# Kernel optimization log

Hardware: AMD Instinct MI355X
Metric: run time of the kernel (lower is better)

Reference implementation:

```python
import jax, jax.numpy as jnp
import numpy as np

N_NODES = 50000
N_EDGES = 800000
IN_CH = 128
HID = 64
OUT_CH = 10
N_GRAPHS = 512


def setup_inputs() -> dict:
    key = jax.random.key(0)
    ks = jax.random.split(key, 16)
    x = jax.random.normal(ks[0], (N_NODES, IN_CH), dtype=jnp.float32)
    edge_index = jax.random.randint(ks[1], (2, N_EDGES), 0, N_NODES, dtype=jnp.int64)
    batch = jnp.sort(jax.random.randint(ks[2], (N_NODES,), 0, N_GRAPHS, dtype=jnp.int64))
    def lin(k, fan_in, fan_out):
        bound = 1.0 / np.sqrt(fan_in)
        kw, kb = jax.random.split(k)
        w = jax.random.uniform(kw, (fan_in, fan_out), minval=-bound, maxval=bound, dtype=jnp.float32)
        b = jax.random.uniform(kb, (fan_out,), minval=-bound, maxval=bound, dtype=jnp.float32)
        return w, b
    w0a, b0a = lin(ks[3], IN_CH, HID)
    w0b, b0b = lin(ks[4], HID, HID)
    w1a, b1a = lin(ks[5], HID, HID)
    w1b, b1b = lin(ks[6], HID, HID)
    fcw, fcb = lin(ks[7], HID, OUT_CH)
    eps0 = jnp.zeros((), dtype=jnp.float32)  # train_eps=True, init 0
    eps1 = jnp.zeros((), dtype=jnp.float32)
    return {"x": x, "edge_index": edge_index, "batch": batch,
            "eps0": eps0, "w0a": w0a, "b0a": b0a, "w0b": w0b, "b0b": b0b,
            "eps1": eps1, "w1a": w1a, "b1a": b1a, "w1b": w1b, "b1b": b1b,
            "fcw": fcw, "fcb": fcb}


def _gin_layer(x, src, dst, eps, wa, ba, wb, bb):
    # sum-aggregate neighbor messages: agg[i] = sum_{(j->i) in E} x[j]
    agg = jax.ops.segment_sum(x[src], dst, num_segments=N_NODES)
    h = (1.0 + eps) * x + agg
    h = jax.nn.relu(h @ wa + ba)
    h = jax.nn.relu(h @ wb + bb)  # MLP ends in ReLU; outer F.relu is a no-op
    return h


def reference(x, edge_index, batch, eps0, w0a, b0a, w0b, b0b,
              eps1, w1a, b1a, w1b, b1b, fcw, fcb):
    src, dst = edge_index[0], edge_index[1]
    h = _gin_layer(x, src, dst, eps0, w0a, b0a, w0b, b0b)
    # dropout skipped (inference)
    h = _gin_layer(h, src, dst, eps1, w1a, b1a, w1b, b1b)
    pooled = jax.ops.segment_sum(h, batch, num_segments=N_GRAPHS)  # [G, HID]
    logits = pooled @ fcw + fcb
    return jax.nn.log_softmax(logits, axis=1)
```

## Files before the change

### kernel.cpp

```cpp
#include <hip/hip_runtime.h>
#include <math.h>

#define IN_CH 128
#define HID 64
#define OUT_CH 10
#define CBLK 512

typedef unsigned int uint32;
typedef unsigned char u8;
typedef unsigned short bf16u;
typedef __attribute__((ext_vector_type(8))) short bf16x8;
typedef __attribute__((ext_vector_type(4))) float f32x4;
typedef __attribute__((ext_vector_type(2))) float f32x2;

static __device__ inline bf16u f2bf(float f) {
    uint32 u = __float_as_uint(f);
    u += 0x7fff + ((u >> 16) & 1);
    return (bf16u)(u >> 16);
}
static __device__ inline uint32 pack2(float a, float b) {
    return (uint32)f2bf(a) | ((uint32)f2bf(b) << 16);
}
static __device__ inline u8 f2fp8(float v) {
    uint32 p = __builtin_amdgcn_cvt_pk_fp8_f32(v, v, 0, false);
    return (u8)(p & 0xff);
}
static __device__ inline void acc_fp8x4(uint32 u, float& a0, float& a1,
                                        float& a2, float& a3) {
    f32x2 lo = __builtin_amdgcn_cvt_pk_f32_fp8((int)u, false);
    f32x2 hi = __builtin_amdgcn_cvt_pk_f32_fp8((int)u, true);
    a0 += lo.x; a1 += lo.y; a2 += hi.x; a3 += hi.y;
}

static __device__ inline void gather_group(
    const uint32* __restrict__ y8, const int* __restrict__ col,
    int rs, int re, int cc,
    float& a0, float& a1, float& a2, float& a3)
{
    int j = rs;
    if (j + 8 <= re) {
        int c0 = col[j],     c1 = col[j + 1], c2 = col[j + 2], c3 = col[j + 3],
            c4 = col[j + 4], c5 = col[j + 5], c6 = col[j + 6], c7 = col[j + 7];
        j += 8;
        while (j + 8 <= re) {
            int n0 = col[j],     n1 = col[j + 1], n2 = col[j + 2], n3 = col[j + 3],
                n4 = col[j + 4], n5 = col[j + 5], n6 = col[j + 6], n7 = col[j + 7];
            uint32 u0 = y8[(long)c0 * 16 + cc], u1 = y8[(long)c1 * 16 + cc],
                   u2 = y8[(long)c2 * 16 + cc], u3 = y8[(long)c3 * 16 + cc],
                   u4 = y8[(long)c4 * 16 + cc], u5 = y8[(long)c5 * 16 + cc],
                   u6 = y8[(long)c6 * 16 + cc], u7 = y8[(long)c7 * 16 + cc];
            acc_fp8x4(u0, a0, a1, a2, a3);
            acc_fp8x4(u1, a0, a1, a2, a3);
            acc_fp8x4(u2, a0, a1, a2, a3);
            acc_fp8x4(u3, a0, a1, a2, a3);
            acc_fp8x4(u4, a0, a1, a2, a3);
            acc_fp8x4(u5, a0, a1, a2, a3);
            acc_fp8x4(u6, a0, a1, a2, a3);
            acc_fp8x4(u7, a0, a1, a2, a3);
            c0 = n0; c1 = n1; c2 = n2; c3 = n3;
            c4 = n4; c5 = n5; c6 = n6; c7 = n7;
            j += 8;
        }
        uint32 u0 = y8[(long)c0 * 16 + cc], u1 = y8[(long)c1 * 16 + cc],
               u2 = y8[(long)c2 * 16 + cc], u3 = y8[(long)c3 * 16 + cc],
               u4 = y8[(long)c4 * 16 + cc], u5 = y8[(long)c5 * 16 + cc],
               u6 = y8[(long)c6 * 16 + cc], u7 = y8[(long)c7 * 16 + cc];
        acc_fp8x4(u0, a0, a1, a2, a3);
        acc_fp8x4(u1, a0, a1, a2, a3);
        acc_fp8x4(u2, a0, a1, a2, a3);
        acc_fp8x4(u3, a0, a1, a2, a3);
        acc_fp8x4(u4, a0, a1, a2, a3);
        acc_fp8x4(u5, a0, a1, a2, a3);
        acc_fp8x4(u6, a0, a1, a2, a3);
        acc_fp8x4(u7, a0, a1, a2, a3);
    }
    for (; j < re; ++j) {
        uint32 u = y8[(long)col[j] * 16 + cc];
        acc_fp8x4(u, a0, a1, a2, a3);
    }
}

__global__ __launch_bounds__(256, 6) void k_pre(
    const int* __restrict__ dst, int* __restrict__ cnt, int* __restrict__ pos,
    const float4* __restrict__ x4, const float* __restrict__ w,
    u8* __restrict__ y, int* __restrict__ wctr, int N, int E)
{
    int tid = threadIdx.x;
    int bid = blockIdx.x;
    if (bid < CBLK) {
        for (int e = bid * 256 + tid; e < E; e += CBLK * 256)
            pos[e] = atomicAdd(&cnt[dst[e]], 1);
    }

    __shared__ __align__(16) uint32 t32[16 * 68];
    __shared__ int sgrp;
    int wid = tid >> 6, lane = tid & 63;
    int quad = lane >> 4, n15 = lane & 15;
    int mycol = wid * 16 + n15;
    bf16x8 fb[4];
    #pragma unroll
    for (int s = 0; s < 4; s++)
        #pragma unroll
        for (int j = 0; j < 8; j++)
            fb[s][j] = (short)f2bf(w[(s * 32 + quad * 8 + j) * HID + mycol]);
    int snode = tid >> 4, sk = tid & 15;
    int NG = (N + 15) >> 4;
    while (true) {
        if (tid == 0) sgrp = atomicAdd(wctr, 1);
        __syncthreads();
        int grp = sgrp;
        if (grp >= NG) break;
        long g0 = (long)grp * 16;
        long node = g0 + snode;
        if (node < N) {
            float4 v0 = x4[node * 32 + sk * 2];
            float4 v1 = x4[node * 32 + sk * 2 + 1];
            uint32 p[4] = {pack2(v0.x, v0.y), pack2(v0.z, v0.w),
                           pack2(v1.x, v1.y), pack2(v1.z, v1.w)};
            *(uint4*)((char*)t32 + snode * 272 + sk * 16) = *(uint4*)p;
        }
        __syncthreads();
        f32x4 acc = {0.f, 0.f, 0.f, 0.f};
        #pragma unroll
        for (int s = 0; s < 4; s++) {
            bf16x8 a = *(const bf16x8*)((const char*)t32 + n15 * 272 + s * 64 + quad * 16);
            acc = __builtin_amdgcn_mfma_f32_16x16x32_bf16(a, fb[s], acc, 0, 0, 0);
        }
        #pragma unroll
        for (int r = 0; r < 4; r++) {
            long n = g0 + quad * 4 + r;
            if (n < N) y[n * HID + mycol] = f2fp8(acc[r]);
        }
        __syncthreads();
    }
}

__global__ __launch_bounds__(256) void k_scan(
    const int* __restrict__ cnt, int* __restrict__ row_ptr,
    int* __restrict__ partials, int* __restrict__ counter, int N, int E, int nch)
{
    __shared__ int red[256];
    int tid = threadIdx.x;
    int bid = blockIdx.x;
    long base = (long)bid * 1024 + tid * 4;
    int v[4]; int s = 0;
    #pragma unroll
    for (int i = 0; i < 4; i++) {
        long idx = base + i;
        v[i] = (idx < N) ? cnt[idx] : 0;
        s += v[i];
    }
    red[tid] = s;
    __syncthreads();
    for (int off = 1; off < 256; off <<= 1) {
        int t = (tid >= off) ? red[tid - off] : 0;
        __syncthreads();
        red[tid] += t;
        __syncthreads();
    }
    int myexcl = red[tid] - s;
    if (tid == 255) {
        __hip_atomic_store(&partials[bid], red[255], __ATOMIC_RELEASE,
                           __HIP_MEMORY_SCOPE_AGENT);
        atomicAdd(counter, 1);
    }
    if (tid == 0) {
        while (__hip_atomic_load(counter, __ATOMIC_ACQUIRE,
                                 __HIP_MEMORY_SCOPE_AGENT) < nch) { }
    }
    __syncthreads();
    int off = 0;
    for (int i = tid; i < bid; i += 256)
        off += __hip_atomic_load(&partials[i], __ATOMIC_RELAXED,
                                 __HIP_MEMORY_SCOPE_AGENT);
    __syncthreads();
    red[tid] = off;
    __syncthreads();
    for (int o = 128; o; o >>= 1) {
        if (tid < o) red[tid] += red[tid + o];
        __syncthreads();
    }
    int run = red[0] + myexcl;
    #pragma unroll
    for (int i = 0; i < 4; i++) {
        long idx = base + i;
        if (idx < N) row_ptr[idx] = run;
        run += v[i];
    }
    if (bid == 0 && tid == 0) row_ptr[N] = E;
}

__global__ __launch_bounds__(256) void k_place(
    const int* __restrict__ src, const int* __restrict__ dst,
    const int* __restrict__ row_ptr, const int* __restrict__ pos,
    int* __restrict__ col, int E)
{
    int e = blockIdx.x * 256 + threadIdx.x;
    if (e >= E) return;
    col[row_ptr[dst[e]] + pos[e]] = src[e];
}

__global__ __launch_bounds__(256, 4) void k_agg0f(
    const uint32* __restrict__ y8, const int* __restrict__ row_ptr,
    const int* __restrict__ col, const float* __restrict__ epsp,
    const float* __restrict__ ba, const float* __restrict__ wb,
    const float* __restrict__ bb, const float* __restrict__ w1a,
    u8* __restrict__ y1, int N)
{
    __shared__ __align__(16) uint32 t32[16 * 36];
    __shared__ __align__(16) uint32 h32[16 * 36];
    int tid = threadIdx.x;
    int wid = tid >> 6, lane = tid & 63;
    int cc = lane & 15, h = lane >> 4;
    int quad = lane >> 4, n15 = lane & 15;
    int n0 = wid * 4;
    int mycol = wid * 16 + n15;
    float e = 1.f + epsp[0];
    float4 bav = ((const float4*)ba)[cc];
    float bbv = bb[mycol];
    bf16x8 fb[2], f1[2];
    #pragma unroll
    for (int s = 0; s < 2; s++)
        #pragma unroll
        for (int j = 0; j < 8; j++) {
            fb[s][j] = (short)f2bf(wb[(s * 32 + quad * 8 + j) * HID + mycol]);
            f1[s][j] = (short)f2bf(w1a[(s * 32 + quad * 8 + j) * HID + mycol]);
        }
    for (long g0 = (long)blockIdx.x * 16; g0 < N; g0 += (long)gridDim.x * 16) {
        long node = g0 + n0 + h;
        if (node < N) {
            int rs = row_ptr[node], re = row_ptr[node + 1];
            uint32 us = y8[node * 16 + cc];
            float a0 = 0.f, a1 = 0.f, a2 = 0.f, a3 = 0.f;
            gather_group(y8, col, rs, re, cc, a0, a1, a2, a3);
            f32x2 lo = __builtin_amdgcn_cvt_pk_f32_fp8((int)us, false);
            f32x2 hi = __builtin_amdgcn_cvt_pk_f32_fp8((int)us, true);
            a0 = fmaf(e, lo.x, a0); a1 = fmaf(e, lo.y, a1);
            a2 = fmaf(e, hi.x, a2); a3 = fmaf(e, hi.y, a3);
            t32[(n0 + h) * 36 + 2 * cc]     = pack2(fmaxf(a0 + bav.x, 0.f),
                                                    fmaxf(a1 + bav.y, 0.f));
            t32[(n0 + h) * 36 + 2 * cc + 1] = pack2(fmaxf(a2 + bav.z, 0.f),
                                                    fmaxf(a3 + bav.w, 0.f));
        }
        __syncthreads();
        f32x4 acc = {bbv, bbv, bbv, bbv};
        {
            bf16x8 a0 = *(const bf16x8*)((const char*)t32 + n15 * 144 + quad * 16);
            bf16x8 a1 = *(const bf16x8*)((const char*)t32 + n15 * 144 + 64 + quad * 16);
            acc = __builtin_amdgcn_mfma_f32_16x16x32_bf16(a0, fb[0], acc, 0, 0, 0);
            acc = __builtin_amdgcn_mfma_f32_16x16x32_bf16(a1, fb[1], acc, 0, 0, 0);
        }
        #pragma unroll
        for (int r = 0; r < 4; r++)
            ((short*)h32)[(quad * 4 + r) * 72 + mycol] = (short)f2bf(fmaxf(acc[r], 0.f));
        __syncthreads();
        f32x4 acc2 = {0.f, 0.f, 0.f, 0.f};
        {
            bf16x8 a0 = *(const bf16x8*)((const char*)h32 + n15 * 144 + quad * 16);
            bf16x8 a1 = *(const bf16x8*)((const char*)h32 + n15 * 144 + 64 + quad * 16);
            acc2 = __builtin_amdgcn_mfma_f32_16x16x32_bf16(a0, f1[0], acc2, 0, 0, 0);
            acc2 = __builtin_amdgcn_mfma_f32_16x16x32_bf16(a1, f1[1], acc2, 0, 0, 0);
        }
        #pragma unroll
        for (int r = 0; r < 4; r++) {
            long n = g0 + quad * 4 + r;
            if (n < N) y1[n * HID + mycol] = f2fp8(acc2[r]);
        }
    }
}

__global__ __launch_bounds__(256, 4) void k_agg1(
    const uint32* __restrict__ y8, const int* __restrict__ row_ptr,
    const int* __restrict__ col, const float* __restrict__ epsp,
    const float* __restrict__ ba, const float* __restrict__ wb,
    const float* __restrict__ bb, const int* __restrict__ batch,
    float* __restrict__ pooled, int N)
{
    __shared__ __align__(16) uint32 t32[16 * 36];
    int tid = threadIdx.x;
    int wid = tid >> 6, lane = tid & 63;
    int cc = lane & 15, h = lane >> 4;
    int quad = lane >> 4, n15 = lane & 15;
    int n0 = wid * 4;
    int mycol = wid * 16 + n15;
    float e = 1.f + epsp[0];
    float4 bav = ((const float4*)ba)[cc];
    float bbv = bb[mycol];
    bf16x8 fb[2];
    #pragma unroll
    for (int s = 0; s < 2; s++)
        #pragma unroll
        for (int j = 0; j < 8; j++)
            fb[s][j] = (short)f2bf(wb[(s * 32 + quad * 8 + j) * HID + mycol]);
    for (long g0 = (long)blockIdx.x * 16; g0 < N; g0 += (long)gridDim.x * 16) {
        long node = g0 + n0 + h;
        if (node < N) {
            int rs = row_ptr[node], re = row_ptr[node + 1];
            uint32 us = y8[node * 16 + cc];
            float a0 = 0.f, a1 = 0.f, a2 = 0.f, a3 = 0.f;
            gather_group(y8, col, rs, re, cc, a0, a1, a2, a3);
            f32x2 lo = __builtin_amdgcn_cvt_pk_f32_fp8((int)us, false);
            f32x2 hi = __builtin_amdgcn_cvt_pk_f32_fp8((int)us, true);
            a0 = fmaf(e, lo.x, a0); a1 = fmaf(e, lo.y, a1);
            a2 = fmaf(e, hi.x, a2); a3 = fmaf(e, hi.y, a3);
            t32[(n0 + h) * 36 + 2 * cc]     = pack2(fmaxf(a0 + bav.x, 0.f),
                                                    fmaxf(a1 + bav.y, 0.f));
            t32[(n0 + h) * 36 + 2 * cc + 1] = pack2(fmaxf(a2 + bav.z, 0.f),
                                                    fmaxf(a3 + bav.w, 0.f));
        }
        __syncthreads();
        f32x4 acc = {bbv, bbv, bbv, bbv};
        {
            bf16x8 a0 = *(const bf16x8*)((const char*)t32 + n15 * 144 + quad * 16);
            bf16x8 a1 = *(const bf16x8*)((const char*)t32 + n15 * 144 + 64 + quad * 16);
            acc = __builtin_amdgcn_mfma_f32_16x16x32_bf16(a0, fb[0], acc, 0, 0, 0);
            acc = __builtin_amdgcn_mfma_f32_16x16x32_bf16(a1, fb[1], acc, 0, 0, 0);
        }
        float rv[4];
        #pragma unroll
        for (int r = 0; r < 4; r++) rv[r] = fmaxf(acc[r], 0.f);
        int nv = (int)((N - g0) < 16 ? (N - g0) : 16);
        int bf_ = batch[g0], bl_ = batch[g0 + nv - 1];
        if (bf_ == bl_) {
            float s = 0.f;
            #pragma unroll
            for (int r = 0; r < 4; r++)
                if (quad * 4 + r < nv) s += rv[r];
            s += __shfl_xor(s, 16);
            s += __shfl_xor(s, 32);
            if (quad == 0)
                atomicAdd(&pooled[(long)bf_ * HID + mycol], s);
        } else {
            #pragma unroll
            for (int r = 0; r < 4; r++) {
                long n = g0 + quad * 4 + r;
                if (n < N)
                    atomicAdd(&pooled[(long)batch[n] * HID + mycol], rv[r]);
            }
        }
        __syncthreads();
    }
}

__global__ __launch_bounds__(64) void k_head(
    const float* __restrict__ pooled, const float* __restrict__ fcw,
    const float* __restrict__ fcb, float* __restrict__ out)
{
    int g = blockIdx.x;
    int l = threadIdx.x;
    float logit = -INFINITY;
    if (l < OUT_CH) {
        float acc = fcb[l];
        #pragma unroll
        for (int k = 0; k < HID; k++)
            acc = fmaf(pooled[g * HID + k], fcw[k * OUT_CH + l], acc);
        logit = acc;
    }
    float m = logit;
    #pragma unroll
    for (int off = 32; off; off >>= 1) m = fmaxf(m, __shfl_xor(m, off));
    float ex = (l < OUT_CH) ? expf(logit - m) : 0.0f;
    float s = ex;
    #pragma unroll
    for (int off = 32; off; off >>= 1) s += __shfl_xor(s, off);
    if (l < OUT_CH) out[g * OUT_CH + l] = logit - m - logf(s);
}

extern "C" void kernel_launch(void* const* d_in, const int* in_sizes, int n_in,
                              void* d_out, int out_size, void* d_ws, size_t ws_size,
                              hipStream_t stream) {
    const float* x    = (const float*)d_in[0];
    const int*   ei   = (const int*)d_in[1];
    const int*   batch= (const int*)d_in[2];
    const float* eps0 = (const float*)d_in[3];
    const float* w0a  = (const float*)d_in[4];
    const float* b0a  = (const float*)d_in[5];
    const float* w0b  = (const float*)d_in[6];
    const float* b0b  = (const float*)d_in[7];
    const float* eps1 = (const float*)d_in[8];
    const float* w1a  = (const float*)d_in[9];
    const float* b1a  = (const float*)d_in[10];
    const float* w1b  = (const float*)d_in[11];
    const float* b1b  = (const float*)d_in[12];
    const float* fcw  = (const float*)d_in[13];
    const float* fcb  = (const float*)d_in[14];
    float* out = (float*)d_out;

    const int N = in_sizes[0] / IN_CH;
    const int E = in_sizes[1] / 2;
    const int G = out_size / OUT_CH;
    const int* src = ei;
    const int* dst = ei + E;

    char* ws = (char*)d_ws;
    int*    row_ptr  = (int*)(ws);
    int*    colv     = (int*)(ws + 200064);
    u8*     y0       = (u8*)(ws + 3400064);
    u8*     y1       = (u8*)(ws + 6600064);
    int*    cnt      = (int*)(ws + 9800064);
    int*    counter  = (int*)(ws + 10000064);
    int*    wctr     = (int*)(ws + 10000068);
    int*    partials = (int*)(ws + 10000128);
    float*  pooled   = (float*)(ws + 10000384);
    int*    pos      = (int*)(ws + 10131456);

    hipMemsetAsync(cnt, 0, 331392, stream);

    int eb = (E + 255) / 256;
    int nb = (N + 31) / 32;
    int nch = (N + 1023) / 1024;
    k_pre<<<nb, 256, 0, stream>>>(dst, cnt, pos, (const float4*)x, w0a, y0,
                                  wctr, N, E);
    k_scan<<<nch, 256, 0, stream>>>(cnt, row_ptr, partials, counter, N, E, nch);
    k_place<<<eb, 256, 0, stream>>>(src, dst, row_ptr, pos, colv, E);

    k_agg0f<<<nb, 256, 0, stream>>>((const uint32*)y0, row_ptr, colv, eps0,
                                    b0a, w0b, b0b, w1a, y1, N);
    k_agg1<<<nb, 256, 0, stream>>>((const uint32*)y1, row_ptr, colv, eps1,
                                   b1a, w1b, b1b, batch, pooled, N);
    k_head<<<G, 64, 0, stream>>>(pooled, fcw, fcb, out);
}
```

Before: 238.1 us.

## Fuse scan and placement kernels, shrink CSR indices to 16-bit, raise occupancy

Merges the prefix-scan and edge placement into one kernel that uses a device-wide spin counter, so non-scan blocks preload their edges while the scan runs. Column and position arrays are stored as 16-bit values, halving gather index traffic. k_pre drops the dynamic work counter in favour of a grid-stride loop and spreads the count atomics across all blocks. The aggregation kernels request higher occupancy. Storing node ids in 16 bits cannot represent N=50000 nodes beyond 65535? It can (50000<65536), but it is fragile for larger graphs. The spin-wait assumes all scan blocks are co-resident.

```diff
diff --git a/kernel.cpp b/kernel.cpp
--- a/kernel.cpp
+++ b/kernel.cpp
@@ -4,10 +4,10 @@
 #define IN_CH 128
 #define HID 64
 #define OUT_CH 10
-#define CBLK 512
 
 typedef unsigned int uint32;
 typedef unsigned char u8;
+typedef unsigned short u16;
 typedef unsigned short bf16u;
 typedef __attribute__((ext_vector_type(8))) short bf16x8;
 typedef __attribute__((ext_vector_type(4))) float f32x4;
@@ -33,7 +33,7 @@
 }
 
 static __device__ inline void gather_group(
-    const uint32* __restrict__ y8, const int* __restrict__ col,
+    const uint32* __restrict__ y8, const u16* __restrict__ col,
     int rs, int re, int cc,
     float& a0, float& a1, float& a2, float& a3)
 {
@@ -81,19 +81,16 @@
 }
 
 __global__ __launch_bounds__(256, 6) void k_pre(
-    const int* __restrict__ dst, int* __restrict__ cnt, int* __restrict__ pos,
+    const int* __restrict__ dst, int* __restrict__ cnt, u16* __restrict__ pos,
     const float4* __restrict__ x4, const float* __restrict__ w,
-    u8* __restrict__ y, int* __restrict__ wctr, int N, int E)
-{
+    u8* __restrict__ y, int N, int E)
+{
+    int gt = blockIdx.x * 256 + threadIdx.x;
+    for (int e = gt; e < E; e += gridDim.x * 256)
+        pos[e] = (u16)atomicAdd(&cnt[dst[e]], 1);
+
+    __shared__ __align__(16) uint32 t32[16 * 68];
     int tid = threadIdx.x;
-    int bid = blockIdx.x;
-    if (bid < CBLK) {
-        for (int e = bid * 256 + tid; e < E; e += CBLK * 256)
-            pos[e] = atomicAdd(&cnt[dst[e]], 1);
-    }
-
-    __shared__ __align__(16) uint32 t32[16 * 68];
-    __shared__ int sgrp;
     int wid = tid >> 6, lane = tid & 63;
     int quad = lane >> 4, n15 = lane & 15;
     int mycol = wid * 16 + n15;
@@ -104,13 +101,7 @@
         for (int j = 0; j < 8; j++)
             fb[s][j] = (short)f2bf(w[(s * 32 + quad * 8 + j) * HID + mycol]);
     int snode = tid >> 4, sk = tid & 15;
-    int NG = (N + 15) >> 4;
-    while (true) {
-        if (tid == 0) sgrp = atomicAdd(wctr, 1);
-        __syncthreads();
-        int grp = sgrp;
-        if (grp >= NG) break;
-        long g0 = (long)grp * 16;
+    for (long g0 = (long)blockIdx.x * 16; g0 < N; g0 += (long)gridDim.x * 16) {
         long node = g0 + snode;
         if (node < N) {
             float4 v0 = x4[node * 32 + sk * 2];
@@ -135,74 +126,106 @@
     }
 }
 
-__global__ __launch_bounds__(256) void k_scan(
+__global__ __launch_bounds__(256) void k_scanplace(
+    const int* __restrict__ src, const int* __restrict__ dst,
     const int* __restrict__ cnt, int* __restrict__ row_ptr,
-    int* __restrict__ partials, int* __restrict__ counter, int N, int E, int nch)
+    const u16* __restrict__ pos, u16* __restrict__ col,
+    int* __restrict__ partials, int* __restrict__ counter,
+    int* __restrict__ counter2, int N, int E, int nch)
 {
     __shared__ int red[256];
     int tid = threadIdx.x;
     int bid = blockIdx.x;
-    long base = (long)bid * 1024 + tid * 4;
-    int v[4]; int s = 0;
-    #pragma unroll
-    for (int i = 0; i < 4; i++) {
-        long idx = base + i;
-        v[i] = (idx < N) ? cnt[idx] : 0;
-        s += v[i];
-    }
-    red[tid] = s;
+    int stride = gridDim.x * 256;
+    int e0 = bid * 256 + tid;
+    int e1 = e0 + stride;
+
+    int d0 = -1, p0 = 0, s0 = 0, d1 = -1, p1 = 0, s1 = 0;
+    if (bid >= nch) {
+        if (e0 < E) { d0 = dst[e0]; p0 = pos[e0]; s0 = src[e0]; }
+        if (e1 < E) { d1 = dst[e1]; p1 = pos[e1]; s1 = src[e1]; }
+    } else {
+        long base = (long)bid * 1024 + tid * 4;
+        int v[4]; int s = 0;
+        #pragma unroll
+        for (int i = 0; i < 4; i++) {
+            long idx = base + i;
+            v[i] = (idx < N) ? cnt[idx] : 0;
+            s += v[i];
+        }
+        red[tid] = s;
+        __syncthreads();
+        for (int off = 1; off < 256; off <<= 1) {
+            int t = (tid >= off) ? red[tid - off] : 0;
+            __syncthreads();
+            red[tid] += t;
+            __syncthreads();
+        }
+        int myexcl = red[tid] - s;
+        if (tid == 255) {
+            __hip_atomic_store(&partials[bid], red[255], __ATOMIC_RELEASE,
+                               __HIP_MEMORY_SCOPE_AGENT);
+            atomicAdd(counter, 1);
+        }
+        if (tid == 0) {
+            while (__hip_atomic_load(counter, __ATOMIC_ACQUIRE,
+                                     __HIP_MEMORY_SCOPE_AGENT) < nch) { }
+        }
+        __syncthreads();
+        int off = 0;
+        for (int i = tid; i < bid; i += 256)
+            off += __hip_atomic_load(&partials[i], __ATOMIC_RELAXED,
+                                     __HIP_MEMORY_SCOPE_AGENT);
+        __syncthreads();
+        red[tid] = off;
+        __syncthreads();
+        for (int o = 128; o; o >>= 1) {
+            if (tid < o) red[tid] += red[tid + o];
+            __syncthreads();
+        }
+        int run = red[0] + myexcl;
+        #pragma unroll
+        for (int i = 0; i < 4; i++) {
+            long idx = base + i;
+            if (idx < N) row_ptr[idx] = run;
+            run += v[i];
+        }
+        if (bid == 0 && tid == 0) row_ptr[N] = E;
+        __syncthreads();
+        if (tid == 0) {
+            __threadfence();
+            atomicAdd(counter2, 1);
+        }
+    }
+
+    if (tid == 0) {
+        while (__hip_atomic_load(counter2, __ATOMIC_ACQUIRE,
+                                 __HIP_MEMORY_SCOPE_AGENT) < nch) { }
+    }
     __syncthreads();
-    for (int off = 1; off < 256; off <<= 1) {
-        int t = (tid >= off) ? red[tid - off] : 0;
-        __syncthreads();
-        red[tid] += t;
-        __syncthreads();
-    }
-    int myexcl = red[tid] - s;
-    if (tid == 255) {
-        __hip_atomic_store(&partials[bid], red[255], __ATOMIC_RELEASE,
-                           __HIP_MEMORY_SCOPE_AGENT);
-        atomicAdd(counter, 1);
-    }
-    if (tid == 0) {
-        while (__hip_atomic_load(counter, __ATOMIC_ACQUIRE,
-                                 __HIP_MEMORY_SCOPE_AGENT) < nch) { }
-    }
-    __syncthreads();
-    int off = 0;
-    for (int i = tid; i < bid; i += 256)
-        off += __hip_atomic_load(&partials[i], __ATOMIC_RELAXED,
-                                 __HIP_MEMORY_SCOPE_AGENT);
-    __syncthreads();
-    red[tid] = off;
-    __syncthreads();
-    for (int o = 128; o; o >>= 1) {
-        if (tid < o) red[tid] += red[tid + o];
-        __syncthreads();
-    }
-    int run = red[0] + myexcl;
-    #pragma unroll
-    for (int i = 0; i < 4; i++) {
-        long idx = base + i;
-        if (idx < N) row_ptr[idx] = run;
-        run += v[i];
-    }
-    if (bid == 0 && tid == 0) row_ptr[N] = E;
-}
-
-__global__ __launch_bounds__(256) void k_place(
-    const int* __restrict__ src, const int* __restrict__ dst,
-    const int* __restrict__ row_ptr, const int* __restrict__ pos,
-    int* __restrict__ col, int E)
-{
-    int e = blockIdx.x * 256 + threadIdx.x;
-    if (e >= E) return;
-    col[row_ptr[dst[e]] + pos[e]] = src[e];
-}
-
-__global__ __launch_bounds__(256, 4) void k_agg0f(
+    if (bid >= nch) {
+        if (d0 >= 0) {
+            int rp = __hip_atomic_load(&row_ptr[d0], __ATOMIC_RELAXED,
+                                       __HIP_MEMORY_SCOPE_AGENT);
+            col[rp + p0] = (u16)s0;
+        }
+        if (d1 >= 0) {
+            int rp = __hip_atomic_load(&row_ptr[d1], __ATOMIC_RELAXED,
+                                       __HIP_MEMORY_SCOPE_AGENT);
+            col[rp + p1] = (u16)s1;
+        }
+    } else {
+        for (int e = e0; e < E; e += stride) {
+            int rp = __hip_atomic_load(&row_ptr[dst[e]], __ATOMIC_RELAXED,
+                                       __HIP_MEMORY_SCOPE_AGENT);
+            col[rp + pos[e]] = (u16)src[e];
+        }
+    }
+}
+
+__global__ __launch_bounds__(256, 6) void k_agg0f(
     const uint32* __restrict__ y8, const int* __restrict__ row_ptr,
-    const int* __restrict__ col, const float* __restrict__ epsp,
+    const u16* __restrict__ col, const float* __restrict__ epsp,
     const float* __restrict__ ba, const float* __restrict__ wb,
     const float* __restrict__ bb, const float* __restrict__ w1a,
     u8* __restrict__ y1, int N)
@@ -269,9 +292,9 @@
     }
 }
 
-__global__ __launch_bounds__(256, 4) void k_agg1(
+__global__ __launch_bounds__(256, 6) void k_agg1(
     const uint32* __restrict__ y8, const int* __restrict__ row_ptr,
-    const int* __restrict__ col, const float* __restrict__ epsp,
+    const u16* __restrict__ col, const float* __restrict__ epsp,
     const float* __restrict__ ba, const float* __restrict__ wb,
     const float* __restrict__ bb, const int* __restrict__ batch,
     float* __restrict__ pooled, int N)
@@ -394,26 +417,23 @@
 
     char* ws = (char*)d_ws;
     int*    row_ptr  = (int*)(ws);
-    int*    colv     = (int*)(ws + 200064);
+    u16*    colv     = (u16*)(ws + 200064);
     u8*     y0       = (u8*)(ws + 3400064);
     u8*     y1       = (u8*)(ws + 6600064);
     int*    cnt      = (int*)(ws + 9800064);
     int*    counter  = (int*)(ws + 10000064);
-    int*    wctr     = (int*)(ws + 10000068);
+    int*    counter2 = (int*)(ws + 10000068);
     int*    partials = (int*)(ws + 10000128);
     float*  pooled   = (float*)(ws + 10000384);
-    int*    pos      = (int*)(ws + 10131456);
+    u16*    pos      = (u16*)(ws + 10131456);
 
     hipMemsetAsync(cnt, 0, 331392, stream);
 
-    int eb = (E + 255) / 256;
     int nb = (N + 31) / 32;
     int nch = (N + 1023) / 1024;
-    k_pre<<<nb, 256, 0, stream>>>(dst, cnt, pos, (const float4*)x, w0a, y0,
-                                  wctr, N, E);
-    k_scan<<<nch, 256, 0, stream>>>(cnt, row_ptr, partials, counter, N, E, nch);
-    k_place<<<eb, 256, 0, stream>>>(src, dst, row_ptr, pos, colv, E);
-
+    k_pre<<<nb, 256, 0, stream>>>(dst, cnt, pos, (const float4*)x, w0a, y0, N, E);
+    k_scanplace<<<nb, 256, 0, stream>>>(src, dst, cnt, row_ptr, pos, colv,
+                                        partials, counter, counter2, N, E, nch);
     k_agg0f<<<nb, 256, 0, stream>>>((const uint32*)y0, row_ptr, colv, eps0,
                                     b0a, w0b, b0b, w1a, y1, N);
     k_agg1<<<nb, 256, 0, stream>>>((const uint32*)y1, row_ptr, colv, eps1,
```

Result: slower. 293.6 us (+23.3%).

## Store CSR column indices as 16-bit and statically schedule pre-kernel

Applied to the files above, without the earlier changes.

Column indices and per-edge positions are narrowed from int32 to uint16, halving index traffic in placement and both aggregation passes. The pre-kernel drops its atomic work-stealing counter in favour of a grid-stride loop over node groups, and spreads the degree-counting atomics over all blocks. Aggregation kernels raise their launch-bounds occupancy hint from 4 to 6. Narrowing to 16 bits cannot hold node ids up to 50000 only if they exceed 65535, so it is valid here but breaks for graphs with more than 65536 nodes or rows of degree above 65535.

```diff
diff --git a/kernel.cpp b/kernel.cpp
--- a/kernel.cpp
+++ b/kernel.cpp
@@ -4,10 +4,10 @@
 #define IN_CH 128
 #define HID 64
 #define OUT_CH 10
-#define CBLK 512
 
 typedef unsigned int uint32;
 typedef unsigned char u8;
+typedef unsigned short u16;
 typedef unsigned short bf16u;
 typedef __attribute__((ext_vector_type(8))) short bf16x8;
 typedef __attribute__((ext_vector_type(4))) float f32x4;
@@ -33,7 +33,7 @@
 }
 
 static __device__ inline void gather_group(
-    const uint32* __restrict__ y8, const int* __restrict__ col,
+    const uint32* __restrict__ y8, const u16* __restrict__ col,
     int rs, int re, int cc,
     float& a0, float& a1, float& a2, float& a3)
 {
@@ -81,19 +81,16 @@
 }
 
 __global__ __launch_bounds__(256, 6) void k_pre(
-    const int* __restrict__ dst, int* __restrict__ cnt, int* __restrict__ pos,
+    const int* __restrict__ dst, int* __restrict__ cnt, u16* __restrict__ pos,
     const float4* __restrict__ x4, const float* __restrict__ w,
-    u8* __restrict__ y, int* __restrict__ wctr, int N, int E)
-{
+    u8* __restrict__ y, int N, int E)
+{
+    int gt = blockIdx.x * 256 + threadIdx.x;
+    for (int e = gt; e < E; e += gridDim.x * 256)
+        pos[e] = (u16)atomicAdd(&cnt[dst[e]], 1);
+
+    __shared__ __align__(16) uint32 t32[16 * 68];
     int tid = threadIdx.x;
-    int bid = blockIdx.x;
-    if (bid < CBLK) {
-        for (int e = bid * 256 + tid; e < E; e += CBLK * 256)
-            pos[e] = atomicAdd(&cnt[dst[e]], 1);
-    }
-
-    __shared__ __align__(16) uint32 t32[16 * 68];
-    __shared__ int sgrp;
     int wid = tid >> 6, lane = tid & 63;
     int quad = lane >> 4, n15 = lane & 15;
     int mycol = wid * 16 + n15;
@@ -104,13 +101,7 @@
         for (int j = 0; j < 8; j++)
             fb[s][j] = (short)f2bf(w[(s * 32 + quad * 8 + j) * HID + mycol]);
     int snode = tid >> 4, sk = tid & 15;
-    int NG = (N + 15) >> 4;
-    while (true) {
-        if (tid == 0) sgrp = atomicAdd(wctr, 1);
-        __syncthreads();
-        int grp = sgrp;
-        if (grp >= NG) break;
-        long g0 = (long)grp * 16;
+    for (long g0 = (long)blockIdx.x * 16; g0 < N; g0 += (long)gridDim.x * 16) {
         long node = g0 + snode;
         if (node < N) {
             float4 v0 = x4[node * 32 + sk * 2];
@@ -192,17 +183,17 @@
 
 __global__ __launch_bounds__(256) void k_place(
     const int* __restrict__ src, const int* __restrict__ dst,
-    const int* __restrict__ row_ptr, const int* __restrict__ pos,
-    int* __restrict__ col, int E)
+    const int* __restrict__ row_ptr, const u16* __restrict__ pos,
+    u16* __restrict__ col, int E)
 {
     int e = blockIdx.x * 256 + threadIdx.x;
     if (e >= E) return;
-    col[row_ptr[dst[e]] + pos[e]] = src[e];
-}
-
-__global__ __launch_bounds__(256, 4) void k_agg0f(
+    col[row_ptr[dst[e]] + pos[e]] = (u16)src[e];
+}
+
+__global__ __launch_bounds__(256, 6) void k_agg0f(
     const uint32* __restrict__ y8, const int* __restrict__ row_ptr,
-    const int* __restrict__ col, const float* __restrict__ epsp,
+    const u16* __restrict__ col, const float* __restrict__ epsp,
     const float* __restrict__ ba, const float* __restrict__ wb,
     const float* __restrict__ bb, const float* __restrict__ w1a,
     u8* __restrict__ y1, int N)
@@ -269,9 +260,9 @@
     }
 }
 
-__global__ __launch_bounds__(256, 4) void k_agg1(
+__global__ __launch_bounds__(256, 6) void k_agg1(
     const uint32* __restrict__ y8, const int* __restrict__ row_ptr,
-    const int* __restrict__ col, const float* __restrict__ epsp,
+    const u16* __restrict__ col, const float* __restrict__ epsp,
     const float* __restrict__ ba, const float* __restrict__ wb,
     const float* __restrict__ bb, const int* __restrict__ batch,
     float* __restrict__ pooled, int N)
@@ -394,23 +385,21 @@
 
     char* ws = (char*)d_ws;
     int*    row_ptr  = (int*)(ws);
-    int*    colv     = (int*)(ws + 200064);
+    u16*    colv     = (u16*)(ws + 200064);
     u8*     y0       = (u8*)(ws + 3400064);
     u8*     y1       = (u8*)(ws + 6600064);
     int*    cnt      = (int*)(ws + 9800064);
     int*    counter  = (int*)(ws + 10000064);
-    int*    wctr     = (int*)(ws + 10000068);
     int*    partials = (int*)(ws + 10000128);
     float*  pooled   = (float*)(ws + 10000384);
-    int*    pos      = (int*)(ws + 10131456);
+    u16*    pos      = (u16*)(ws + 10131456);
 
     hipMemsetAsync(cnt, 0, 331392, stream);
 
     int eb = (E + 255) / 256;
     int nb = (N + 31) / 32;
     int nch = (N + 1023) / 1024;
-    k_pre<<<nb, 256, 0, stream>>>(dst, cnt, pos, (const float4*)x, w0a, y0,
-                                  wctr, N, E);
+    k_pre<<<nb, 256, 0, stream>>>(dst, cnt, pos, (const float4*)x, w0a, y0, N, E);
     k_scan<<<nch, 256, 0, stream>>>(cnt, row_ptr, partials, counter, N, E, nch);
     k_place<<<eb, 256, 0, stream>>>(src, dst, row_ptr, pos, colv, E);
 
```

After: 208.4 us. 12.5% less time.
